# Optimization experiments

Hardware: AMD Instinct MI355X
Metric: run time of the kernel (lower is better)

The kernel has to match this reference:

```python
import jax, jax.numpy as jnp
import numpy as np
import math

B, N = 1, 768
CS, CZ, CH, H, PQ, PV, E3 = 384, 128, 16, 12, 4, 8, 4
INF, EPS = 1e5, 1e-8


def _quat_to_rot(q):
    # q: [..., 4] unnormalized quaternion -> [..., 3, 3] rotation matrix
    q = q / jnp.linalg.norm(q, axis=-1, keepdims=True)
    w, x, y, z = q[..., 0], q[..., 1], q[..., 2], q[..., 3]
    R = jnp.stack([
        1 - 2 * (y * y + z * z), 2 * (x * y - w * z), 2 * (x * z + w * y),
        2 * (x * y + w * z), 1 - 2 * (x * x + z * z), 2 * (y * z - w * x),
        2 * (x * z - w * y), 2 * (y * z + w * x), 1 - 2 * (x * x + y * y),
    ], axis=-1)
    return R.reshape(q.shape[:-1] + (3, 3))


def setup_inputs() -> dict:
    key = jax.random.key(0)
    ks = jax.random.split(key, 24)
    hc = H * CH
    hpq = H * PQ * 3
    hpkv = H * (PQ + PV) * 3
    cod = CZ // 4 + CH + PV * 4  # 80
    def w(k, shape, fan_in):
        return jax.random.normal(k, shape, jnp.float32) / math.sqrt(fan_in)
    inp = {
        "s": jax.random.normal(ks[0], (B, N, CS), jnp.float32),
        "z": jax.random.normal(ks[1], (B, N, N, CZ), jnp.float32),
        "l1_feats": jax.random.normal(ks[2], (B, N, E3 * 3), jnp.float32),
        "rot": _quat_to_rot(jax.random.normal(ks[3], (B, N, 4), jnp.float32)),
        "trans": jax.random.normal(ks[4], (B, N, 3), jnp.float32),
        "mask": jnp.ones((B, N), jnp.float32),
        "Wq": w(ks[5], (hc, CS), CS), "bq": jnp.zeros((hc,), jnp.float32),
        "Wkv": w(ks[6], (2 * hc, CS), CS), "bkv": jnp.zeros((2 * hc,), jnp.float32),
        "Wqp": w(ks[7], (hpq, CS), CS), "bqp": jnp.zeros((hpq,), jnp.float32),
        "Wkvp": w(ks[8], (hpkv, CS), CS), "bkvp": jnp.zeros((hpkv,), jnp.float32),
        "Wb": w(ks[9], (H, CZ), CZ), "bb": jnp.zeros((H,), jnp.float32),
        "Wdz": w(ks[10], (CZ // 4, CZ), CZ), "bdz": jnp.zeros((CZ // 4,), jnp.float32),
        "Wout": w(ks[11], (CS, H * cod), H * cod), "bout": jnp.zeros((CS,), jnp.float32),
        "Wl1": jax.random.normal(ks[12], (H * PV, E3), jnp.float32),
    }
    return inp


def _split3(x):
    # torch.split(x, d//3, -1) then stack(dim=-1): [..., 3*P] -> [..., P, 3]
    return jnp.swapaxes(x.reshape(x.shape[:-1] + (3, -1)), -1, -2)


def reference(s, z, l1_feats, rot, trans, mask,
              Wq, bq, Wkv, bkv, Wqp, bqp, Wkvp, bkvp,
              Wb, bb, Wdz, bdz, Wout, bout, Wl1):
    s_org = s
    q = (s @ Wq.T + bq).reshape(B, N, H, CH)
    kv = (s @ Wkv.T + bkv).reshape(B, N, H, 2 * CH)
    k, v = kv[..., :CH], kv[..., CH:]

    # points in global frame: R p + t
    q_pts = _split3(s @ Wqp.T + bqp)                      # [B,N,H*PQ,3]
    q_pts = jnp.einsum("bnij,bnpj->bnpi", rot, q_pts) + trans[:, :, None, :]
    q_pts = q_pts.reshape(B, N, H, PQ, 3)
    kv_pts = _split3(s @ Wkvp.T + bkvp)                   # [B,N,H*(PQ+PV),3]
    kv_pts = jnp.einsum("bnij,bnpj->bnpi", rot, kv_pts) + trans[:, :, None, :]
    kv_pts = kv_pts.reshape(B, N, H, PQ + PV, 3)
    k_pts, v_pts = kv_pts[..., :PQ, :], kv_pts[..., PQ:, :]

    b = z @ Wb.T + bb                                     # [B,N,N,H]
    a = math.sqrt(1.0 / (3 * CH)) * jnp.einsum("bihc,bjhc->bhij", q, k)
    a = a + math.sqrt(1.0 / 3) * jnp.transpose(b, (0, 3, 1, 2))

    diff = q_pts[:, :, None] - k_pts[:, None]             # [B,N,N,H,PQ,3]
    pt_att = -0.5 * jnp.sum(diff * diff, axis=(-1, -2))   # [B,N,N,H]
    a = a + jnp.transpose(pt_att, (0, 3, 1, 2))

    sq_mask = INF * (mask[:, :, None] * mask[:, None, :] - 1.0)
    a = jax.nn.softmax(a + sq_mask[:, None], axis=-1)     # [B,H,N,N]

    o = jnp.einsum("bhij,bjhc->bihc", a, v).reshape(B, N, H * CH)
    o_pt = jnp.einsum("bhij,bjhpc->bihpc", a, v_pts)      # [B,N,H,PV,3] (global frame)

    # e3nn o3.Linear on (H*PV)x1o -> E3x1o: per-xyz channel mixing / sqrt(fan_in)
    o_pt_l1 = o_pt.reshape(B, N, H * PV, 3)
    l1_out = l1_feats + (jnp.einsum("bnic,io->bnoc", o_pt_l1, Wl1)
                         / math.sqrt(H * PV)).reshape(B, N, E3 * 3)

    # back to local frame: R^T (p - t)
    o_pt_loc = jnp.einsum("bnji,bnhpj->bnhpi", rot,
                          o_pt - trans[:, :, None, None, :])
    o_pt_dists = jnp.sqrt(jnp.sum(o_pt_loc ** 2, axis=-1) + EPS).reshape(B, N, H * PV)
    o_pt_flat = o_pt_loc.reshape(B, N, H * PV, 3)

    pair_z = z @ Wdz.T + bdz                              # [B,N,N,CZ//4]
    o_pair = jnp.einsum("bhij,bijd->bihd", a, pair_z).reshape(B, N, H * (CZ // 4))

    feats = jnp.concatenate([o, o_pt_flat[..., 0], o_pt_flat[..., 1],
                             o_pt_flat[..., 2], o_pt_dists, o_pair], axis=-1)
    s_out = feats @ Wout.T + bout + s_org
    return s_out, l1_out
```

## Files before the change

kernel.cpp:

```cpp
#include <hip/hip_runtime.h>

#define INFV 100000.0f
#define CQK 0.14433756729740643f
#define SQCQK 0.3799178428257963f
#define CB  0.5773502691896258f
#define INV_SQRT96 0.10206207261596577f

typedef short bf16x8 __attribute__((ext_vector_type(8)));
typedef float f32x4 __attribute__((ext_vector_type(4)));

#define OFF_WT    0
#define OFF_WOT   442368
#define OFF_BU    811008
#define OFF_BM    1328256
#define OFF_A     4867200
#define OFF_VCT   8406144
#define OFF_PZ    8627328
#define OFF_O     18064512
#define OFF_OPT   18211968
#define OFF_OPAIR 18433152
#define OFF_ZB    18728064
#define OFF_WC    18728068
#define OFF_BC    18731140
#define OFF_QC    18731200
#define OFF_KC    19026112
#define OFF_SQK   19321024

static __device__ __forceinline__ unsigned short f2bf(float x) {
  unsigned int u = __float_as_uint(x);
  unsigned int r = (u + 0x7fffu + ((u >> 16) & 1u)) >> 16;
  return (unsigned short)r;
}
static __device__ __forceinline__ float bf2f(unsigned short b) {
  return __uint_as_float(((unsigned int)b) << 16);
}

__global__ __launch_bounds__(256) void kT(
    const float* __restrict__ Wq, const float* __restrict__ Wkv,
    const float* __restrict__ Wqp, const float* __restrict__ Wkvp,
    const float* __restrict__ Wout,
    const float* __restrict__ bq, const float* __restrict__ bkv,
    const float* __restrict__ bqp, const float* __restrict__ bkvp,
    const float* __restrict__ Wb, const float* __restrict__ bb,
    const float* __restrict__ Wdz, const float* __restrict__ bdz,
    float* __restrict__ WT, float* __restrict__ WoutT, float* __restrict__ bu,
    unsigned short* __restrict__ vcT, float* __restrict__ zb,
    unsigned short* __restrict__ Wc, float* __restrict__ biasc) {
  int tid = blockIdx.x * 256 + threadIdx.x;
  if (tid < 442368) {
    int f = tid / 1152, u = tid % 1152;
    float w;
    if (u < 192)      w = Wq[u * 384 + f];
    else if (u < 576) w = Wkv[(u - 192) * 384 + f];
    else if (u < 720) w = Wqp[(u - 576) * 384 + f];
    else              w = Wkvp[(u - 720) * 384 + f];
    WT[tid] = w;
  } else if (tid < 811008) {
    int r = tid - 442368;
    int f = r / 384, o = r % 384;
    WoutT[r] = Wout[o * 960 + f];
  } else if (tid < 812160) {
    int u = tid - 811008;
    float bv;
    if (u < 192)      bv = bq[u];
    else if (u < 576) bv = bkv[u - 192];
    else if (u < 720) bv = bqp[u - 576];
    else              bv = bkvp[u - 720];
    bu[u] = bv;
  } else if (tid < 849024) {
    int zid = tid - 812160;
    int h = zid / 3072, r = zid % 3072;
    ((unsigned int*)(vcT + h * 36864 + 40 * 768))[r] = 0u;
  } else if (tid < 849028) {
    ((unsigned int*)zb)[tid - 849024] = 0u;
  } else if (tid < 855172) {
    int wid = tid - 849028;
    int n = wid >> 7, k = wid & 127;
    float val = (n < 12) ? CB * Wb[n * 128 + k] : ((n < 44) ? Wdz[(n - 12) * 128 + k] : 0.f);
    Wc[wid] = f2bf(val);
  } else if (tid < 855220) {
    int n = tid - 855172;
    biasc[n] = (n < 12) ? CB * bb[n] : ((n < 44) ? bdz[n - 12] : 0.f);
  }
}

__global__ __launch_bounds__(384) void kA(
    const float* __restrict__ s, const float* __restrict__ rot, const float* __restrict__ trans,
    const float* __restrict__ WT, const float* __restrict__ bu,
    unsigned short* __restrict__ qc, unsigned short* __restrict__ kc,
    float* __restrict__ sqk, unsigned short* __restrict__ vcT) {
  __shared__ float sA[4][384];
  __shared__ float praw[4][576];
  __shared__ float sqp[4][12][4];
  const int t = threadIdx.x;
  const int n0 = blockIdx.x * 4;
  for (int idx = t; idx < 4 * 384; idx += 384) sA[idx / 384][idx % 384] = s[n0 * 384 + idx];
  __syncthreads();

  float acc[3][4];
#pragma unroll
  for (int a = 0; a < 3; a++)
#pragma unroll
    for (int r = 0; r < 4; r++) acc[a][r] = 0.f;
  const int u0 = t, u1 = t + 384, u2 = t + 768;

  for (int f = 0; f < 384; f += 4) {
    float4 sr0 = *(const float4*)&sA[0][f];
    float4 sr1 = *(const float4*)&sA[1][f];
    float4 sr2 = *(const float4*)&sA[2][f];
    float4 sr3 = *(const float4*)&sA[3][f];
#pragma unroll
    for (int ff = 0; ff < 4; ff++) {
      const float* wrow = WT + (size_t)(f + ff) * 1152;
      float w0 = wrow[u0], w1 = wrow[u1], w2 = wrow[u2];
      float v0 = ((const float*)&sr0)[ff];
      float v1 = ((const float*)&sr1)[ff];
      float v2 = ((const float*)&sr2)[ff];
      float v3 = ((const float*)&sr3)[ff];
      acc[0][0] = fmaf(w0, v0, acc[0][0]); acc[0][1] = fmaf(w0, v1, acc[0][1]);
      acc[0][2] = fmaf(w0, v2, acc[0][2]); acc[0][3] = fmaf(w0, v3, acc[0][3]);
      acc[1][0] = fmaf(w1, v0, acc[1][0]); acc[1][1] = fmaf(w1, v1, acc[1][1]);
      acc[1][2] = fmaf(w1, v2, acc[1][2]); acc[1][3] = fmaf(w1, v3, acc[1][3]);
      acc[2][0] = fmaf(w2, v0, acc[2][0]); acc[2][1] = fmaf(w2, v1, acc[2][1]);
      acc[2][2] = fmaf(w2, v2, acc[2][2]); acc[2][3] = fmaf(w2, v3, acc[2][3]);
    }
  }

#pragma unroll
  for (int a = 0; a < 3; a++) {
    int u = t + a * 384;
    float bv = bu[u];
#pragma unroll
    for (int r = 0; r < 4; r++) {
      float val = acc[a][r] + bv;
      int n = n0 + r;
      if (u < 192) {
        int h = u >> 4, c = u & 15;
        qc[((size_t)(h * 768) + n) * 64 + c] = f2bf(SQCQK * val);
      } else if (u < 576) {
        int l2 = u - 192, h = l2 >> 5, rem = l2 & 31;
        if (rem < 16) kc[((size_t)(h * 768) + n) * 64 + rem] = f2bf(SQCQK * val);
        else          vcT[h * 36864 + (rem - 16) * 768 + n] = f2bf(val);
      } else {
        praw[r][u - 576] = val;
      }
    }
  }
  __syncthreads();

  for (int task = t; task < 768; task += 384) {
    int r = task / 192, rem = task % 192;
    int h = rem >> 4, pidx = rem & 15;
    int n = n0 + r;
    const float* R = rot + n * 9;
    const float* tr = trans + n * 3;
    float x, y, z;
    if (pidx < 4) {
      int p = h * 4 + pidx;
      x = praw[r][p]; y = praw[r][48 + p]; z = praw[r][96 + p];
    } else {
      int pp = h * 12 + (pidx - 4);
      x = praw[r][144 + pp]; y = praw[r][288 + pp]; z = praw[r][432 + pp];
    }
    float g0 = R[0] * x + R[1] * y + R[2] * z + tr[0];
    float g1 = R[3] * x + R[4] * y + R[5] * z + tr[1];
    float g2 = R[6] * x + R[7] * y + R[8] * z + tr[2];
    if (pidx < 4) {
      unsigned short* base = qc + ((size_t)(h * 768) + n) * 64;
      int d0 = 16 + pidx * 3;
      float g[3] = {g0, g1, g2};
#pragma unroll
      for (int c = 0; c < 3; c++) {
        unsigned short hi = f2bf(g[c]);
        unsigned short lo = f2bf(g[c] - bf2f(hi));
        base[d0 + c] = hi; base[12 + d0 + c] = lo; base[24 + d0 + c] = hi;
      }
    } else if (pidx < 8) {
      unsigned short* base = kc + ((size_t)(h * 768) + n) * 64;
      int d0 = 16 + (pidx - 4) * 3;
      float g[3] = {g0, g1, g2};
#pragma unroll
      for (int c = 0; c < 3; c++) {
        unsigned short hi = f2bf(g[c]);
        unsigned short lo = f2bf(g[c] - bf2f(hi));
        base[d0 + c] = hi; base[12 + d0 + c] = hi; base[24 + d0 + c] = lo;
      }
      sqp[r][h][pidx - 4] = g0 * g0 + g1 * g1 + g2 * g2;
    } else {
      int pv = pidx - 8;
      unsigned short* vb = vcT + h * 36864 + (16 + pv * 3) * 768 + n;
      vb[0] = f2bf(g0); vb[768] = f2bf(g1); vb[1536] = f2bf(g2);
    }
  }
  for (int task = t; task < 576; task += 384) {
    int r = task / 144, rem = task % 144;
    int h = rem / 12, c = rem % 12;
    size_t off = ((size_t)(h * 768) + n0 + r) * 64 + 52 + c;
    qc[off] = 0; kc[off] = 0;
  }
  __syncthreads();
  if (t < 48) {
    int r = t / 12, h = t % 12;
    sqk[h * 768 + n0 + r] = sqp[r][h][0] + sqp[r][h][1] + sqp[r][h][2] + sqp[r][h][3];
  }
}

__global__ __launch_bounds__(256) void kB4(
    const float* __restrict__ z, const unsigned short* __restrict__ Wc,
    const float* __restrict__ biasc,
    unsigned short* __restrict__ bm16, unsigned short* __restrict__ pzT) {
  __shared__ unsigned short zL[64][136];
  __shared__ unsigned short wL[48][136];
  __shared__ unsigned short oD[64][49];
  __shared__ float biasL[48];
  const int t = threadIdx.x;
  const size_t pid0 = (size_t)blockIdx.x * 64;
  const int iRow = blockIdx.x / 12;
  const int j0 = (blockIdx.x % 12) * 64;

  {
    const unsigned int* wsrc = (const unsigned int*)Wc;
#pragma unroll
    for (int it = 0; it < 12; it++) {
      int idx = it * 256 + t;
      int n = idx >> 6, col = (idx & 63) * 2;
      *(unsigned int*)&wL[n][col] = wsrc[idx];
    }
    if (t < 48) biasL[t] = biasc[t];
  }
  const float4* zsrc = (const float4*)(z + pid0 * 128);
#pragma unroll
  for (int it = 0; it < 8; it++) {
    int f4 = it * 256 + t;
    float4 v = zsrc[f4];
    int row = f4 >> 5, col = (f4 & 31) * 4;
    unsigned int p0 = (unsigned int)f2bf(v.x) | ((unsigned int)f2bf(v.y) << 16);
    unsigned int p1 = (unsigned int)f2bf(v.z) | ((unsigned int)f2bf(v.w) << 16);
    uint2 pk = make_uint2(p0, p1);
    *(uint2*)&zL[row][col] = pk;
  }
  __syncthreads();

  const int w = t >> 6, l = t & 63;
  const int lr = l & 15, hk = l >> 4;
  f32x4 acc0 = {0.f, 0.f, 0.f, 0.f}, acc1 = acc0, acc2 = acc0;
  const int arow = w * 16 + lr;
#pragma unroll
  for (int kc = 0; kc < 4; kc++) {
    int col = kc * 32 + hk * 8;
    bf16x8 af = *(const bf16x8*)&zL[arow][col];
    bf16x8 b0 = *(const bf16x8*)&wL[lr][col];
    bf16x8 b1 = *(const bf16x8*)&wL[16 + lr][col];
    bf16x8 b2 = *(const bf16x8*)&wL[32 + lr][col];
    acc0 = __builtin_amdgcn_mfma_f32_16x16x32_bf16(af, b0, acc0, 0, 0, 0);
    acc1 = __builtin_amdgcn_mfma_f32_16x16x32_bf16(af, b1, acc1, 0, 0, 0);
    acc2 = __builtin_amdgcn_mfma_f32_16x16x32_bf16(af, b2, acc2, 0, 0, 0);
  }
  {
    int rb = w * 16 + hk * 4;
#pragma unroll
    for (int r = 0; r < 4; r++) {
      oD[rb + r][lr]      = f2bf(acc0[r] + biasL[lr]);
      oD[rb + r][16 + lr] = f2bf(acc1[r] + biasL[16 + lr]);
      oD[rb + r][32 + lr] = f2bf(acc2[r] + biasL[32 + lr]);
    }
  }
  __syncthreads();

  {
    int d = t >> 3, jc = t & 7;
    union { unsigned short u[8]; uint4 v; } pk;
#pragma unroll
    for (int e = 0; e < 8; e++) pk.u[e] = oD[jc * 8 + e][12 + d];
    *(uint4*)(pzT + ((size_t)iRow * 32 + d) * 768 + j0 + jc * 8) = pk.v;
  }
  for (int idx = t; idx < 384; idx += 256) {
    int h = idx / 32, pr = idx % 32;
    unsigned int u = (unsigned int)oD[2 * pr][h] | ((unsigned int)oD[2 * pr + 1][h] << 16);
    ((unsigned int*)(bm16 + (size_t)h * 589824 + pid0))[pr] = u;
  }
}

__global__ __launch_bounds__(256) void kC1M(
    const unsigned short* __restrict__ qc, const unsigned short* __restrict__ kc,
    const float* __restrict__ sqk, const unsigned short* __restrict__ bm16,
    const float* __restrict__ mask, unsigned short* __restrict__ A) {
  __shared__ float lg[16 * 780];
  const int t = threadIdx.x;
  const int h = blockIdx.x % 12, it = blockIdx.x / 12;
  const int i0 = it * 16;
  const int w = t >> 6, l = t & 63;
  const int lr = l & 15, hk = l >> 4;

  const unsigned short* qrow = qc + ((size_t)(h * 768) + i0 + lr) * 64 + hk * 8;
  bf16x8 a0 = *(const bf16x8*)(qrow);
  bf16x8 a1 = *(const bf16x8*)(qrow + 32);
  float miA[4];
#pragma unroll
  for (int r = 0; r < 4; r++) miA[r] = mask[i0 + hk * 4 + r];

  for (int q = 0; q < 12; q++) {
    int j0 = (w * 12 + q) * 16;
    const unsigned short* krow = kc + ((size_t)(h * 768) + j0 + lr) * 64 + hk * 8;
    bf16x8 b0 = *(const bf16x8*)(krow);
    bf16x8 b1 = *(const bf16x8*)(krow + 32);
    f32x4 acc = {0.f, 0.f, 0.f, 0.f};
    acc = __builtin_amdgcn_mfma_f32_16x16x32_bf16(a0, b0, acc, 0, 0, 0);
    acc = __builtin_amdgcn_mfma_f32_16x16x32_bf16(a1, b1, acc, 0, 0, 0);
    int j = j0 + lr;
    float skj = 0.5f * sqk[h * 768 + j];
    float mj = mask[j];
    const unsigned short* bmc = bm16 + (size_t)h * 589824 + (size_t)(i0 + hk * 4) * 768 + j;
#pragma unroll
    for (int r = 0; r < 4; r++) {
      int ii = hk * 4 + r;
      float bsc = bf2f(bmc[r * 768]);
      lg[ii * 780 + j] = acc[r] - skj + bsc + INFV * (miA[r] * mj - 1.0f);
    }
  }
  __syncthreads();

  const int ln = l;
#pragma unroll
  for (int rr = 0; rr < 4; rr++) {
    int row = w * 4 + rr;
    float* rowp = lg + row * 780;
    float m = -3.0e38f;
#pragma unroll
    for (int kq = 0; kq < 12; kq++) m = fmaxf(m, rowp[ln + kq * 64]);
#pragma unroll
    for (int sh = 1; sh < 64; sh <<= 1) m = fmaxf(m, __shfl_xor(m, sh));
    float ssum = 0.f;
#pragma unroll
    for (int kq = 0; kq < 12; kq++) ssum += __expf(rowp[ln + kq * 64] - m);
#pragma unroll
    for (int sh = 1; sh < 64; sh <<= 1) ssum += __shfl_xor(ssum, sh);
    float iv = 1.0f / ssum;
    unsigned int* arow = (unsigned int*)(A + (size_t)h * 589824 + (size_t)(i0 + row) * 768);
#pragma unroll
    for (int kq = 0; kq < 6; kq++) {
      int jp = ln + kq * 64;
      float e0 = __expf(rowp[2 * jp] - m) * iv;
      float e1 = __expf(rowp[2 * jp + 1] - m) * iv;
      arow[jp] = (unsigned int)f2bf(e0) | ((unsigned int)f2bf(e1) << 16);
    }
  }
}

__global__ __launch_bounds__(128) void kC2(
    const unsigned short* __restrict__ A, const unsigned short* __restrict__ vcT,
    float* __restrict__ o_out, float* __restrict__ opt_out) {
  const int t = threadIdx.x;
  const int h = blockIdx.x % 12, it = blockIdx.x / 12;
  const int i0 = it * 32;
  const int w = t >> 6, l = t & 63;
  const int lr = l & 15, lk = (l >> 4) * 8;
  f32x4 acc0 = {0.f, 0.f, 0.f, 0.f}, acc1 = acc0, acc2 = acc0;
  const unsigned short* ab = A + (size_t)h * 589824 + (i0 + w * 16 + lr) * 768 + lk;
  const unsigned short* bb = vcT + h * 36864 + lr * 768 + lk;
#pragma unroll 4
  for (int kc = 0; kc < 24; kc++) {
    int k0 = kc * 32;
    bf16x8 avf = *(const bf16x8*)(ab + k0);
    bf16x8 b0 = *(const bf16x8*)(bb + k0);
    bf16x8 b1 = *(const bf16x8*)(bb + 16 * 768 + k0);
    bf16x8 b2 = *(const bf16x8*)(bb + 32 * 768 + k0);
    acc0 = __builtin_amdgcn_mfma_f32_16x16x32_bf16(avf, b0, acc0, 0, 0, 0);
    acc1 = __builtin_amdgcn_mfma_f32_16x16x32_bf16(avf, b1, acc1, 0, 0, 0);
    acc2 = __builtin_amdgcn_mfma_f32_16x16x32_bf16(avf, b2, acc2, 0, 0, 0);
  }
  const int rowb = i0 + w * 16 + (l >> 4) * 4;
#pragma unroll
  for (int r = 0; r < 4; r++) {
    int row = rowb + r;
    o_out[row * 192 + h * 16 + lr] = acc0[r];
    opt_out[row * 288 + h * 24 + lr] = acc1[r];
    if (lr < 8) opt_out[row * 288 + h * 24 + 16 + lr] = acc2[r];
  }
}

__global__ __launch_bounds__(256) void kC3b(
    const unsigned short* __restrict__ A, const unsigned short* __restrict__ pzT,
    const unsigned short* __restrict__ zb, float* __restrict__ opair_out) {
  __shared__ float red[4][16][33];
  const int t = threadIdx.x, i = blockIdx.x;
  const int w = t >> 6, l = t & 63;
  const int lr = l & 15, lk = (l >> 4) * 8;
  f32x4 acc0 = {0.f, 0.f, 0.f, 0.f}, acc1 = acc0;
  const unsigned short* abase = (lr < 12) ? (A + (size_t)lr * 589824 + i * 768 + lk) : zb;
  const int astep = (lr < 12) ? 1 : 0;
  const unsigned short* pz0 = pzT + ((size_t)i * 32 + lr) * 768 + lk;
  const unsigned short* pz1 = pzT + ((size_t)i * 32 + 16 + lr) * 768 + lk;
#pragma unroll
  for (int kc = 0; kc < 6; kc++) {
    int k0 = w * 192 + kc * 32;
    bf16x8 avf = *(const bf16x8*)(abase + astep * k0);
    bf16x8 b0 = *(const bf16x8*)(pz0 + k0);
    bf16x8 b1 = *(const bf16x8*)(pz1 + k0);
    acc0 = __builtin_amdgcn_mfma_f32_16x16x32_bf16(avf, b0, acc0, 0, 0, 0);
    acc1 = __builtin_amdgcn_mfma_f32_16x16x32_bf16(avf, b1, acc1, 0, 0, 0);
  }
#pragma unroll
  for (int r = 0; r < 4; r++) {
    red[w][(l >> 4) * 4 + r][lr] = acc0[r];
    red[w][(l >> 4) * 4 + r][16 + lr] = acc1[r];
  }
  __syncthreads();
  for (int idx = t; idx < 512; idx += 256) {
    int row = idx >> 5, col = idx & 31;
    if (row < 12) {
      float sv = red[0][row][col] + red[1][row][col] + red[2][row][col] + red[3][row][col];
      opair_out[i * 384 + row * 32 + col] = sv;
    }
  }
}

__global__ __launch_bounds__(512) void kD(
    const float* __restrict__ o_in, const float* __restrict__ opt_in, const float* __restrict__ opair_in,
    const float* __restrict__ rot, const float* __restrict__ trans,
    const float* __restrict__ l1f, const float* __restrict__ Wl1,
    const float* __restrict__ WoutT, const float* __restrict__ bout,
    const float* __restrict__ s_org, float* __restrict__ out) {
  __shared__ float feats[4][960];
  __shared__ float part[2][256][6];
  const int t = threadIdx.x;
  const int n0 = blockIdx.x * 4;

  for (int idx = t; idx < 768; idx += 512) feats[idx / 192][idx % 192] = o_in[n0 * 192 + idx];
  for (int idx = t; idx < 1536; idx += 512) feats[idx / 384][576 + idx % 384] = opair_in[n0 * 384 + idx];
  if (t < 384) {
    int r = t / 96, p = t % 96, n = n0 + r;
    float x = opt_in[n * 288 + p * 3 + 0];
    float y = opt_in[n * 288 + p * 3 + 1];
    float zc = opt_in[n * 288 + p * 3 + 2];
    const float* R = rot + n * 9;
    const float* tr = trans + n * 3;
    float dx = x - tr[0], dy = y - tr[1], dz = zc - tr[2];
    float l0 = R[0] * dx + R[3] * dy + R[6] * dz;
    float l1 = R[1] * dx + R[4] * dy + R[7] * dz;
    float l2 = R[2] * dx + R[5] * dy + R[8] * dz;
    feats[r][192 + p] = l0;
    feats[r][288 + p] = l1;
    feats[r][384 + p] = l2;
    feats[r][480 + p] = sqrtf(l0 * l0 + l1 * l1 + l2 * l2 + 1e-8f);
  } else if (t < 432) {
    int tt = t - 384, r = tt / 12, lq = tt % 12, n = n0 + r;
    int oo = lq / 3, cc = lq % 3;
    float acc = 0.f;
    for (int i = 0; i < 96; i++) acc = fmaf(opt_in[n * 288 + i * 3 + cc], Wl1[i * 4 + oo], acc);
    out[294912 + n * 12 + lq] = l1f[n * 12 + lq] + acc * INV_SQRT96;
  }
  __syncthreads();

  const int fh = t >> 8, tt = t & 255;
  const int o0 = tt & 127, rp = tt >> 7;
  float acc[3][2] = {{0.f, 0.f}, {0.f, 0.f}, {0.f, 0.f}};
  for (int f = fh * 480; f < fh * 480 + 480; f++) {
    float w0 = WoutT[f * 384 + o0];
    float w1 = WoutT[f * 384 + o0 + 128];
    float w2 = WoutT[f * 384 + o0 + 256];
    float s0 = feats[rp * 2][f], s1 = feats[rp * 2 + 1][f];
    acc[0][0] = fmaf(w0, s0, acc[0][0]); acc[0][1] = fmaf(w0, s1, acc[0][1]);
    acc[1][0] = fmaf(w1, s0, acc[1][0]); acc[1][1] = fmaf(w1, s1, acc[1][1]);
    acc[2][0] = fmaf(w2, s0, acc[2][0]); acc[2][1] = fmaf(w2, s1, acc[2][1]);
  }
#pragma unroll
  for (int kq = 0; kq < 3; kq++)
#pragma unroll
    for (int r = 0; r < 2; r++) part[fh][tt][kq * 2 + r] = acc[kq][r];
  __syncthreads();
  if (t < 256) {
    const int ob = t & 127, rb = t >> 7;
#pragma unroll
    for (int kq = 0; kq < 3; kq++) {
      int o = ob + kq * 128;
#pragma unroll
      for (int r = 0; r < 2; r++) {
        int n = n0 + rb * 2 + r;
        float v = part[0][t][kq * 2 + r] + part[1][t][kq * 2 + r] + bout[o] + s_org[n * 384 + o];
        out[n * 384 + o] = v;
      }
    }
  }
}

extern "C" void kernel_launch(void* const* d_in, const int* in_sizes, int n_in,
                              void* d_out, int out_size, void* d_ws, size_t ws_size,
                              hipStream_t stream) {
  (void)in_sizes; (void)n_in; (void)out_size; (void)ws_size;
  const float* s     = (const float*)d_in[0];
  const float* z     = (const float*)d_in[1];
  const float* l1f   = (const float*)d_in[2];
  const float* rot   = (const float*)d_in[3];
  const float* trans = (const float*)d_in[4];
  const float* mask  = (const float*)d_in[5];
  const float* Wq    = (const float*)d_in[6];
  const float* bq    = (const float*)d_in[7];
  const float* Wkv   = (const float*)d_in[8];
  const float* bkv   = (const float*)d_in[9];
  const float* Wqp   = (const float*)d_in[10];
  const float* bqp   = (const float*)d_in[11];
  const float* Wkvp  = (const float*)d_in[12];
  const float* bkvp  = (const float*)d_in[13];
  const float* Wb    = (const float*)d_in[14];
  const float* bb    = (const float*)d_in[15];
  const float* Wdz   = (const float*)d_in[16];
  const float* bdz   = (const float*)d_in[17];
  const float* Wout  = (const float*)d_in[18];
  const float* bout  = (const float*)d_in[19];
  const float* Wl1   = (const float*)d_in[20];
  float* out = (float*)d_out;
  float* ws  = (float*)d_ws;

  float* WT    = ws + OFF_WT;
  float* WoutT = ws + OFF_WOT;
  float* bu    = ws + OFF_BU;
  unsigned short* bm16 = (unsigned short*)(ws + OFF_BM);
  unsigned short* Ab   = (unsigned short*)(ws + OFF_A);
  unsigned short* vcT  = (unsigned short*)(ws + OFF_VCT);
  unsigned short* pzTb = (unsigned short*)(ws + OFF_PZ);
  float* ob    = ws + OFF_O;
  float* optb  = ws + OFF_OPT;
  float* opairb= ws + OFF_OPAIR;
  float* zbf   = ws + OFF_ZB;
  unsigned short* Wc = (unsigned short*)(ws + OFF_WC);
  float* biasc = ws + OFF_BC;
  unsigned short* qcb = (unsigned short*)(ws + OFF_QC);
  unsigned short* kcb = (unsigned short*)(ws + OFF_KC);
  float* sqkb = ws + OFF_SQK;

  kT<<<3342, 256, 0, stream>>>(Wq, Wkv, Wqp, Wkvp, Wout, bq, bkv, bqp, bkvp,
                               Wb, bb, Wdz, bdz,
                               WT, WoutT, bu, vcT, zbf, Wc, biasc);
  kA<<<192, 384, 0, stream>>>(s, rot, trans, WT, bu, qcb, kcb, sqkb, vcT);
  kB4<<<9216, 256, 0, stream>>>(z, Wc, biasc, bm16, pzTb);
  kC1M<<<576, 256, 0, stream>>>(qcb, kcb, sqkb, bm16, mask, Ab);
  kC2<<<288, 128, 0, stream>>>(Ab, vcT, ob, optb);
  kC3b<<<768, 256, 0, stream>>>(Ab, pzTb, (const unsigned short*)zbf, opairb);
  kD<<<192, 512, 0, stream>>>(ob, optb, opairb, rot, trans, l1f, Wl1, WoutT, bout, s, out);
}
```

Measured before the change: 230.6 us.

## Read z-projection weights from global directly and split A·V over K across warps

The z-projection kernel no longer stages the small weight matrix and bias in shared memory. Each lane now loads its B fragments straight from global or L2 and keeps the bias in registers, which drops the LDS fill and cuts LDS use so more blocks can be resident. The A·V kernel is reshaped into a split-K form: each 256-thread block handles 16 rows, the four warps each cover a quarter of the 768-long K dimension, and the partial results are summed in shared memory. This doubles the grid to 576 blocks for better occupancy, at the cost of an extra reduction pass and barrier.

```diff
diff --git a/kernel.cpp b/kernel.cpp
--- a/kernel.cpp
+++ b/kernel.cpp
@@ -205,29 +205,19 @@
   }
 }
 
-__global__ __launch_bounds__(256) void kB4(
+__global__ __launch_bounds__(256) void kB5(
     const float* __restrict__ z, const unsigned short* __restrict__ Wc,
     const float* __restrict__ biasc,
     unsigned short* __restrict__ bm16, unsigned short* __restrict__ pzT) {
   __shared__ unsigned short zL[64][136];
-  __shared__ unsigned short wL[48][136];
   __shared__ unsigned short oD[64][49];
-  __shared__ float biasL[48];
   const int t = threadIdx.x;
   const size_t pid0 = (size_t)blockIdx.x * 64;
   const int iRow = blockIdx.x / 12;
   const int j0 = (blockIdx.x % 12) * 64;
-
-  {
-    const unsigned int* wsrc = (const unsigned int*)Wc;
-#pragma unroll
-    for (int it = 0; it < 12; it++) {
-      int idx = it * 256 + t;
-      int n = idx >> 6, col = (idx & 63) * 2;
-      *(unsigned int*)&wL[n][col] = wsrc[idx];
-    }
-    if (t < 48) biasL[t] = biasc[t];
-  }
+  const int w = t >> 6, l = t & 63;
+  const int lr = l & 15, hk = l >> 4;
+
   const float4* zsrc = (const float4*)(z + pid0 * 128);
 #pragma unroll
   for (int it = 0; it < 8; it++) {
@@ -239,19 +229,18 @@
     uint2 pk = make_uint2(p0, p1);
     *(uint2*)&zL[row][col] = pk;
   }
-  __syncthreads();
-
-  const int w = t >> 6, l = t & 63;
-  const int lr = l & 15, hk = l >> 4;
+  const float b0f = biasc[lr], b1f = biasc[16 + lr], b2f = biasc[32 + lr];
+  __syncthreads();
+
   f32x4 acc0 = {0.f, 0.f, 0.f, 0.f}, acc1 = acc0, acc2 = acc0;
   const int arow = w * 16 + lr;
 #pragma unroll
   for (int kc = 0; kc < 4; kc++) {
     int col = kc * 32 + hk * 8;
     bf16x8 af = *(const bf16x8*)&zL[arow][col];
-    bf16x8 b0 = *(const bf16x8*)&wL[lr][col];
-    bf16x8 b1 = *(const bf16x8*)&wL[16 + lr][col];
-    bf16x8 b2 = *(const bf16x8*)&wL[32 + lr][col];
+    bf16x8 b0 = *(const bf16x8*)(Wc + (size_t)lr * 128 + col);
+    bf16x8 b1 = *(const bf16x8*)(Wc + (size_t)(16 + lr) * 128 + col);
+    bf16x8 b2 = *(const bf16x8*)(Wc + (size_t)(32 + lr) * 128 + col);
     acc0 = __builtin_amdgcn_mfma_f32_16x16x32_bf16(af, b0, acc0, 0, 0, 0);
     acc1 = __builtin_amdgcn_mfma_f32_16x16x32_bf16(af, b1, acc1, 0, 0, 0);
     acc2 = __builtin_amdgcn_mfma_f32_16x16x32_bf16(af, b2, acc2, 0, 0, 0);
@@ -260,9 +249,9 @@
     int rb = w * 16 + hk * 4;
 #pragma unroll
     for (int r = 0; r < 4; r++) {
-      oD[rb + r][lr]      = f2bf(acc0[r] + biasL[lr]);
-      oD[rb + r][16 + lr] = f2bf(acc1[r] + biasL[16 + lr]);
-      oD[rb + r][32 + lr] = f2bf(acc2[r] + biasL[32 + lr]);
+      oD[rb + r][lr]      = f2bf(acc0[r] + b0f);
+      oD[rb + r][16 + lr] = f2bf(acc1[r] + b1f);
+      oD[rb + r][32 + lr] = f2bf(acc2[r] + b2f);
     }
   }
   __syncthreads();
@@ -347,20 +336,21 @@
   }
 }
 
-__global__ __launch_bounds__(128) void kC2(
+__global__ __launch_bounds__(256) void kC2b(
     const unsigned short* __restrict__ A, const unsigned short* __restrict__ vcT,
     float* __restrict__ o_out, float* __restrict__ opt_out) {
+  __shared__ float red[4][16][49];
   const int t = threadIdx.x;
   const int h = blockIdx.x % 12, it = blockIdx.x / 12;
-  const int i0 = it * 32;
+  const int i0 = it * 16;
   const int w = t >> 6, l = t & 63;
   const int lr = l & 15, lk = (l >> 4) * 8;
   f32x4 acc0 = {0.f, 0.f, 0.f, 0.f}, acc1 = acc0, acc2 = acc0;
-  const unsigned short* ab = A + (size_t)h * 589824 + (i0 + w * 16 + lr) * 768 + lk;
+  const unsigned short* ab = A + (size_t)h * 589824 + (size_t)(i0 + lr) * 768 + lk;
   const unsigned short* bb = vcT + h * 36864 + lr * 768 + lk;
-#pragma unroll 4
-  for (int kc = 0; kc < 24; kc++) {
-    int k0 = kc * 32;
+#pragma unroll
+  for (int kc = 0; kc < 6; kc++) {
+    int k0 = w * 192 + kc * 32;
     bf16x8 avf = *(const bf16x8*)(ab + k0);
     bf16x8 b0 = *(const bf16x8*)(bb + k0);
     bf16x8 b1 = *(const bf16x8*)(bb + 16 * 768 + k0);
@@ -369,13 +359,20 @@
     acc1 = __builtin_amdgcn_mfma_f32_16x16x32_bf16(avf, b1, acc1, 0, 0, 0);
     acc2 = __builtin_amdgcn_mfma_f32_16x16x32_bf16(avf, b2, acc2, 0, 0, 0);
   }
-  const int rowb = i0 + w * 16 + (l >> 4) * 4;
+  const int rb = (l >> 4) * 4;
 #pragma unroll
   for (int r = 0; r < 4; r++) {
-    int row = rowb + r;
-    o_out[row * 192 + h * 16 + lr] = acc0[r];
-    opt_out[row * 288 + h * 24 + lr] = acc1[r];
-    if (lr < 8) opt_out[row * 288 + h * 24 + 16 + lr] = acc2[r];
+    red[w][rb + r][lr] = acc0[r];
+    red[w][rb + r][16 + lr] = acc1[r];
+    red[w][rb + r][32 + lr] = acc2[r];
+  }
+  __syncthreads();
+  for (int idx = t; idx < 768; idx += 256) {
+    int row = idx / 48, c = idx % 48;
+    float sv = red[0][row][c] + red[1][row][c] + red[2][row][c] + red[3][row][c];
+    int gr = i0 + row;
+    if (c < 16)      o_out[gr * 192 + h * 16 + c] = sv;
+    else if (c < 40) opt_out[gr * 288 + h * 24 + (c - 16)] = sv;
   }
 }
 
@@ -533,9 +530,9 @@
                                Wb, bb, Wdz, bdz,
                                WT, WoutT, bu, vcT, zbf, Wc, biasc);
   kA<<<192, 384, 0, stream>>>(s, rot, trans, WT, bu, qcb, kcb, sqkb, vcT);
-  kB4<<<9216, 256, 0, stream>>>(z, Wc, biasc, bm16, pzTb);
+  kB5<<<9216, 256, 0, stream>>>(z, Wc, biasc, bm16, pzTb);
   kC1M<<<576, 256, 0, stream>>>(qcb, kcb, sqkb, bm16, mask, Ab);
-  kC2<<<288, 128, 0, stream>>>(Ab, vcT, ob, optb);
+  kC2b<<<576, 256, 0, stream>>>(Ab, vcT, ob, optb);
   kC3b<<<768, 256, 0, stream>>>(Ab, pzTb, (const unsigned short*)zbf, opairb);
   kD<<<192, 512, 0, stream>>>(ob, optb, opairb, rot, trans, l1f, Wl1, WoutT, bout, s, out);
 }
```

Result: slower. 240.7 us (+4.4%).
